# Kernel optimization log

Hardware: AMD Instinct MI355X
Metric: run time of the kernel (lower is better)

## Reference

```python
import jax, jax.numpy as jnp
import numpy as np
from jax import lax

K = 5          # CARAFE kernel_size
S = 2          # scale_factor (downsample stride)
GROUP = 1      # mask groups
ENC_PAD = 1    # (encoder_kernel-1)*dilation//2 with encoder_kernel=3


def _conv2d(x, w, b, stride, padding, dilation=1):
    y = lax.conv_general_dilated(
        x, w, window_strides=(stride, stride),
        padding=[(padding, padding), (padding, padding)],
        rhs_dilation=(dilation, dilation),
        dimension_numbers=('NCHW', 'OIHW', 'NCHW'))
    return y + b[None, :, None, None]


def setup_inputs() -> dict:
    key = jax.random.key(0)
    k1, k2, k3 = jax.random.split(key, 3)
    B, C, H, W = 4, 256, 128, 128
    COMP = 64
    x = jax.random.normal(k1, (B, C, H, W), dtype=jnp.float32)
    # xavier-uniform-ish scale for compressor, std=0.001 for content encoder (as in init_weights)
    w1 = jax.random.normal(k2, (COMP, C, 1, 1), dtype=jnp.float32) * (1.0 / np.sqrt(C))
    b1 = jnp.zeros((COMP,), dtype=jnp.float32)
    w2 = jax.random.normal(k3, (K * K * GROUP, COMP, 3, 3), dtype=jnp.float32) * 0.001
    b2 = jnp.zeros((K * K * GROUP,), dtype=jnp.float32)
    return {"x": x, "w1": w1, "b1": b1, "w2": w2, "b2": b2}


def _carafe_forward(x, w1, b1, w2, b2):
    B, C, H, W = x.shape
    compressed = _conv2d(x, w1, b1, stride=1, padding=0)           # (B, 64, H, W)
    mask = _conv2d(compressed, w2, b2, stride=S, padding=ENC_PAD)   # (B, K*K*G, Ho, Wo)
    Ho, Wo = mask.shape[2], mask.shape[3]
    # kernel_normalizer: softmax over the K*K window per group
    mask = jax.nn.softmax(mask.reshape(B, GROUP, K * K, Ho, Wo), axis=2)
    # feature_reassemble: fused unfold * mask sum — accumulate per kernel tap to
    # avoid materializing the full (B, C, K*K, Ho, Wo) tensor.
    pad = K // 2
    x_pad = jnp.pad(x, ((0, 0), (0, 0), (pad, pad), (pad, pad)))
    Cg = C // GROUP
    out = jnp.zeros((B, GROUP, Cg, Ho, Wo), dtype=x.dtype)
    for i in range(K):
        for j in range(K):
            patch = x_pad[:, :, i:i + S * (Ho - 1) + 1:S, j:j + S * (Wo - 1) + 1:S]
            patch = patch.reshape(B, GROUP, Cg, Ho, Wo)
            out = out + patch * mask[:, :, i * K + j][:, :, None]
    return out.reshape(B, C, Ho, Wo)


def reference(x, w1, b1, w2, b2):
    return _carafe_forward(x, w1, b1, w2, b2)
```

## Files before the change

### kernel.cpp

```cpp
#include <hip/hip_runtime.h>
#include <math.h>

#define BN   4
#define CN   256
#define HN   128
#define WN   128
#define COMP 64
#define KK   25
#define HO   64
#define WO   64

#define TB_OFF    36864
#define XT_OFF    37120
#define WS_NEED   ((size_t)(XT_OFF + (size_t)BN * HN * WN * CN / 2) * 4)

typedef short v8s  __attribute__((ext_vector_type(8)));
typedef float v16f __attribute__((ext_vector_type(16)));

__device__ inline ushort f2bf(float f) {
  unsigned u = __float_as_uint(f);
  return (ushort)((u + 0x7fffu + ((u >> 16) & 1u)) >> 16);
}

__global__ __launch_bounds__(256) void prep_kernel(
    const float* __restrict__ x, const float* __restrict__ w1,
    const float* __restrict__ b1, const float* __restrict__ w2,
    float* __restrict__ ws) {
  const int bid = blockIdx.x;
  const int tid = threadIdx.x;
  if (bid < 4096) {
    __shared__ float st[64][65];
    const int b = bid >> 10, h = (bid >> 3) & 127, bx = bid & 7;
    const int wt = bx & 1, ct = bx >> 1;
    const int w0 = wt * 64, c0 = ct * 64;
    {
      const int wl = tid & 63, cw = tid >> 6;
#pragma unroll
      for (int i = 0; i < 16; ++i) {
        int cl = cw * 16 + i;
        st[cl][wl] = x[((size_t)(b * CN + c0 + cl) * HN + h) * WN + w0 + wl];
      }
    }
    __syncthreads();
    ushort* xT = (ushort*)(ws + XT_OFF);
    const int cg = tid & 15, wl0 = tid >> 4;
#pragma unroll
    for (int wi = 0; wi < 4; ++wi) {
      int wl = wl0 + wi * 16;
      ushort4 o = make_ushort4(f2bf(st[cg * 4 + 0][wl]), f2bf(st[cg * 4 + 1][wl]),
                               f2bf(st[cg * 4 + 2][wl]), f2bf(st[cg * 4 + 3][wl]));
      *(ushort4*)(xT + ((size_t)((b * HN + h) * WN + w0 + wl)) * CN + c0 + cg * 4) = o;
    }
  } else {
    const int cid = bid - 4096;
    const int t = cid >> 2;
    const int chunk = (cid & 3) * 4 + (tid >> 6);
    const int lane = tid & 63;
    const int m = lane & 31, half = lane >> 5;
    const int c0 = chunk * 16 + half * 8;
    float acc[8] = {0.f, 0.f, 0.f, 0.f, 0.f, 0.f, 0.f, 0.f};
    if (m < KK) {
      for (int k = 0; k < COMP; ++k) {
        float wv = w2[(size_t)(m * COMP + k) * 9 + t];
        const float* w1r = w1 + (size_t)k * CN + c0;
        float4 a = *(const float4*)w1r;
        float4 bq = *(const float4*)(w1r + 4);
        acc[0] += wv * a.x;  acc[1] += wv * a.y;
        acc[2] += wv * a.z;  acc[3] += wv * a.w;
        acc[4] += wv * bq.x; acc[5] += wv * bq.y;
        acc[6] += wv * bq.z; acc[7] += wv * bq.w;
      }
    }
    ushort* wA = (ushort*)ws;
    ushort pk[8];
#pragma unroll
    for (int j = 0; j < 8; ++j) pk[j] = f2bf(acc[j]);
    *(ushort4*)(wA + ((size_t)(t * 16 + chunk) * 64 + lane) * 8) =
        make_ushort4(pk[0], pk[1], pk[2], pk[3]);
    *(ushort4*)(wA + ((size_t)(t * 16 + chunk) * 64 + lane) * 8 + 4) =
        make_ushort4(pk[4], pk[5], pk[6], pk[7]);
    if (chunk == 0 && lane < KK) {
      float tbv = 0.f;
      for (int k = 0; k < COMP; ++k)
        tbv += w2[(size_t)(lane * COMP + k) * 9 + t] * b1[k];
      ws[TB_OFF + lane * 9 + t] = tbv;
    }
  }
}

__global__ __launch_bounds__(1024, 4) void conv_softmax_gather(
    const float* __restrict__ ws, const float* __restrict__ b2,
    const float* __restrict__ x, float* __restrict__ out) {
  const int ho = blockIdx.x, b = blockIdx.y;
  const int tid = threadIdx.x;
  const int lane = tid & 63;
  const int wv = tid >> 6;
  const int n = lane & 31, half = lane >> 5;
  const ushort* xT = (const ushort*)(ws + XT_OFF);
  const ushort* wA = (const ushort*)ws;
  const int coff = wv * 16 + half * 8;
  const v8s zero8 = {};
  v16f acc[2] = {{}, {}};

  __shared__ float red[8 * KK * 64];
  __shared__ float sml[KK * 64];

#pragma unroll
  for (int dr = 0; dr < 3; ++dr) {
    const int r = 2 * ho + dr - 1;
    if (r < 0) continue;
#pragma unroll
    for (int dc = 0; dc < 3; ++dc) {
      const int t = dr * 3 + dc;
      const ushort* ap = wA + ((size_t)(t * 16 + wv) * 64 + lane) * 8;
      v8s af = *(const v8s*)ap;
      const size_t rowbase = (size_t)((b * HN + r) * WN);
#pragma unroll
      for (int wt = 0; wt < 2; ++wt) {
        const int wo = wt * 32 + n;
        const int q = 2 * wo + dc - 1;
        const bool bad = q < 0;
        const int qc = bad ? 0 : q;
        const ushort* bp = xT + (rowbase + qc) * CN + coff;
        v8s bf = *(const v8s*)bp;
        if (dc == 0 && bad) bf = zero8;
        acc[wt] = __builtin_amdgcn_mfma_f32_32x32x16_bf16(af, bf, acc[wt], 0, 0, 0);
      }
    }
  }

  const int wo = lane;
  const int c_base = __builtin_amdgcn_readfirstlane(wv * 16);
  const float* __restrict__ xb = x + (size_t)(b * CN) * (HN * WN);
  const int col = 2 * wo;
  float2 g[2][5];
  auto load_g = [&](int ci, float2* dst) {
    const float* xc = xb + (size_t)(c_base + ci) * (HN * WN);
#pragma unroll
    for (int i = 0; i < 5; ++i) {
      int r = 2 * ho - 2 + i;
      dst[i] = (r >= 0 && r < HN) ? *(const float2*)(xc + r * WN + col)
                                  : make_float2(0.f, 0.f);
    }
  };
  load_g(0, g[0]);
  load_g(1, g[1]);

  if (wv >= 8) {
#pragma unroll
    for (int wt = 0; wt < 2; ++wt)
#pragma unroll
      for (int rg = 0; rg < 16; ++rg) {
        int m = (rg & 3) + 8 * (rg >> 2) + 4 * half;
        if (m < KK) red[((wv - 8) * KK + m) * 64 + wt * 32 + n] = acc[wt][rg];
      }
  }
  __syncthreads();
  if (wv < 8) {
#pragma unroll
    for (int wt = 0; wt < 2; ++wt)
#pragma unroll
      for (int rg = 0; rg < 16; ++rg) {
        int m = (rg & 3) + 8 * (rg >> 2) + 4 * half;
        if (m < KK) red[(wv * KK + m) * 64 + wt * 32 + n] += acc[wt][rg];
      }
  }
  __syncthreads();
  if (wv < 4) {
#pragma unroll
    for (int m = 0; m < KK; ++m)
      red[(wv * KK + m) * 64 + wo] += red[((wv + 4) * KK + m) * 64 + wo];
  }
  __syncthreads();
  if (wv < 2) {
#pragma unroll
    for (int m = 0; m < KK; ++m)
      red[(wv * KK + m) * 64 + wo] += red[((wv + 2) * KK + m) * 64 + wo];
  }
  __syncthreads();
  if (tid < 64) {
    const float* tb = ws + TB_OFF;
    const float vr0 = (ho > 0) ? 1.f : 0.f;
    const float vq0 = (wo > 0) ? 1.f : 0.f;
    float logit[KK];
    float mx = -1e30f;
#pragma unroll
    for (int m = 0; m < KK; ++m) {
      const float* t9 = tb + m * 9;
      float l = b2[m]
              + vr0 * (vq0 * t9[0] + t9[1] + t9[2])
              +       (vq0 * t9[3] + t9[4] + t9[5])
              +       (vq0 * t9[6] + t9[7] + t9[8]);
      l += red[(0 * KK + m) * 64 + wo] + red[(1 * KK + m) * 64 + wo];
      logit[m] = l;
      mx = fmaxf(mx, l);
    }
    float ssum = 0.f;
#pragma unroll
    for (int m = 0; m < KK; ++m) {
      float e = __expf(logit[m] - mx);
      logit[m] = e;
      ssum += e;
    }
    float inv = 1.f / ssum;
#pragma unroll
    for (int m = 0; m < KK; ++m) sml[m * 64 + wo] = logit[m] * inv;
  }
  __syncthreads();

  float smr[KK];
#pragma unroll
  for (int m = 0; m < KK; ++m) smr[m] = sml[m * 64 + wo];

  const float wok = (wo > 0) ? 1.f : 0.f;
  const float w63 = (wo < 63) ? 1.f : 0.f;
  for (int ci = 0; ci < 16; ++ci) {
    float2 v[5];
#pragma unroll
    for (int i = 0; i < 5; ++i) v[i] = g[ci & 1][i];
    if (ci + 2 < 16) load_g(ci + 2, g[ci & 1]);

    float acc2 = 0.f;
#pragma unroll
    for (int i = 0; i < 5; ++i) {
      float lx = wok * __shfl_up(v[i].x, 1, 64);
      float ly = wok * __shfl_up(v[i].y, 1, 64);
      float rx = w63 * __shfl_down(v[i].x, 1, 64);
      acc2 += lx * smr[i * 5 + 0] + ly * smr[i * 5 + 1]
            + v[i].x * smr[i * 5 + 2] + v[i].y * smr[i * 5 + 3]
            + rx * smr[i * 5 + 4];
    }
    out[(((size_t)(b * CN + c_base + ci)) * HO + ho) * WO + wo] = acc2;
  }
}

#define FB_WSTRIDE 240
#define FB_TB_OFF  (256 * FB_WSTRIDE)

__global__ __launch_bounds__(256) void compose_w_fb(
    const float* __restrict__ w1, const float* __restrict__ b1,
    const float* __restrict__ w2, float* __restrict__ ws) {
  int mt = blockIdx.x, c = threadIdx.x;
  float acc = 0.f;
#pragma unroll 8
  for (int k = 0; k < COMP; ++k)
    acc += w2[(size_t)(mt / 9 * COMP + k) * 9 + (mt % 9)] * w1[k * CN + c];
  ws[c * FB_WSTRIDE + mt] = acc;
  if (mt < FB_WSTRIDE - 225) ws[c * FB_WSTRIDE + 225 + mt] = 0.f;
  if (c == 0) {
    float tbv = 0.f;
    for (int k = 0; k < COMP; ++k)
      tbv += w2[(size_t)(mt / 9 * COMP + k) * 9 + (mt % 9)] * b1[k];
    ws[FB_TB_OFF + mt] = tbv;
  }
}

__global__ __launch_bounds__(1024, 4) void fused_fb(
    const float* __restrict__ x, const float* __restrict__ b2,
    const float* __restrict__ ws, float* __restrict__ out) {
  const int ho = blockIdx.x, b = blockIdx.y, tid = threadIdx.x;
  const int wo = tid & 63, wv = tid >> 6;
  const int c_base = __builtin_amdgcn_readfirstlane(wv * 16);
  const float* __restrict__ w2c = ws;
  const float* __restrict__ tb  = ws + FB_TB_OFF;
  __shared__ float red[8 * KK * 64];
  __shared__ float sm[KK * 64];
  const float* __restrict__ xb = x + (size_t)(b * CN) * (HN * WN);
  const int col = 2 * wo;
  float acc[KK];
#pragma unroll
  for (int m = 0; m < KK; ++m) acc[m] = 0.f;
  float2 xbuf[2][3];
  auto load_ch = [&](int ci, float2* dst) {
    const float* xc = xb + (size_t)(c_base + ci) * (HN * WN);
    dst[0] = (ho > 0) ? *(const float2*)(xc + (2 * ho - 1) * WN + col)
                      : make_float2(0.f, 0.f);
    dst[1] = *(const float2*)(xc + (2 * ho) * WN + col);
    dst[2] = *(const float2*)(xc + (2 * ho + 1) * WN + col);
  };
  load_ch(0, xbuf[0]);
  load_ch(1, xbuf[1]);
  const float wok = (wo > 0) ? 1.f : 0.f;
  for (int ci = 0; ci < 16; ++ci) {
    float2 r0 = xbuf[ci & 1][0], r1 = xbuf[ci & 1][1], r2 = xbuf[ci & 1][2];
    if (ci + 2 < 16) load_ch(ci + 2, xbuf[ci & 1]);
    float xv[9];
    xv[0] = wok * __shfl_up(r0.y, 1, 64); xv[1] = r0.x; xv[2] = r0.y;
    xv[3] = wok * __shfl_up(r1.y, 1, 64); xv[4] = r1.x; xv[5] = r1.y;
    xv[6] = wok * __shfl_up(r2.y, 1, 64); xv[7] = r2.x; xv[8] = r2.y;
    const float* __restrict__ wrow = w2c + (size_t)(c_base + ci) * FB_WSTRIDE;
#pragma unroll
    for (int m = 0; m < KK; ++m) {
      float a = acc[m];
#pragma unroll
      for (int t = 0; t < 9; ++t) a += wrow[m * 9 + t] * xv[t];
      acc[m] = a;
    }
  }
  float2 g[2][5];
  auto load_g = [&](int ci, float2* dst) {
    const float* xc = xb + (size_t)(c_base + ci) * (HN * WN);
#pragma unroll
    for (int i = 0; i < 5; ++i) {
      int r = 2 * ho - 2 + i;
      dst[i] = (r >= 0 && r < HN) ? *(const float2*)(xc + r * WN + col)
                                  : make_float2(0.f, 0.f);
    }
  };
  load_g(0, g[0]);
  load_g(1, g[1]);
  if (wv >= 8) {
#pragma unroll
    for (int m = 0; m < KK; ++m) red[((wv - 8) * KK + m) * 64 + wo] = acc[m];
  }
  __syncthreads();
  if (wv < 8) {
#pragma unroll
    for (int m = 0; m < KK; ++m) red[(wv * KK + m) * 64 + wo] += acc[m];
  }
  __syncthreads();
  if (wv < 4) {
#pragma unroll
    for (int m = 0; m < KK; ++m)
      red[(wv * KK + m) * 64 + wo] += red[((wv + 4) * KK + m) * 64 + wo];
  }
  __syncthreads();
  if (wv < 2) {
#pragma unroll
    for (int m = 0; m < KK; ++m)
      red[(wv * KK + m) * 64 + wo] += red[((wv + 2) * KK + m) * 64 + wo];
  }
  __syncthreads();
  if (tid < 64) {
    const float vr0 = (ho > 0) ? 1.f : 0.f;
    const float vq0 = (wo > 0) ? 1.f : 0.f;
    float logit[KK];
    float mx = -1e30f;
#pragma unroll
    for (int m = 0; m < KK; ++m) {
      const float* t9 = tb + m * 9;
      float l = b2[m]
              + vr0 * (vq0 * t9[0] + t9[1] + t9[2])
              +       (vq0 * t9[3] + t9[4] + t9[5])
              +       (vq0 * t9[6] + t9[7] + t9[8]);
      l += red[(0 * KK + m) * 64 + wo] + red[(1 * KK + m) * 64 + wo];
      logit[m] = l;
      mx = fmaxf(mx, l);
    }
    float s = 0.f;
#pragma unroll
    for (int m = 0; m < KK; ++m) {
      float e = __expf(logit[m] - mx);
      logit[m] = e;
      s += e;
    }
    float inv = 1.f / s;
#pragma unroll
    for (int m = 0; m < KK; ++m) sm[m * 64 + wo] = logit[m] * inv;
  }
  __syncthreads();
  float smr[KK];
#pragma unroll
  for (int m = 0; m < KK; ++m) smr[m] = sm[m * 64 + wo];
  const float w63 = (wo < 63) ? 1.f : 0.f;
  for (int ci = 0; ci < 16; ++ci) {
    float2 v[5];
#pragma unroll
    for (int i = 0; i < 5; ++i) v[i] = g[ci & 1][i];
    if (ci + 2 < 16) load_g(ci + 2, g[ci & 1]);
    float acc2 = 0.f;
#pragma unroll
    for (int i = 0; i < 5; ++i) {
      float lx = wok * __shfl_up(v[i].x, 1, 64);
      float ly = wok * __shfl_up(v[i].y, 1, 64);
      float rx = w63 * __shfl_down(v[i].x, 1, 64);
      acc2 += lx * smr[i * 5 + 0] + ly * smr[i * 5 + 1]
            + v[i].x * smr[i * 5 + 2] + v[i].y * smr[i * 5 + 3]
            + rx * smr[i * 5 + 4];
    }
    out[(((size_t)(b * CN + c_base + ci)) * HO + ho) * WO + wo] = acc2;
  }
}

extern "C" void kernel_launch(void* const* d_in, const int* in_sizes, int n_in,
                              void* d_out, int out_size, void* d_ws, size_t ws_size,
                              hipStream_t stream) {
  const float* x  = (const float*)d_in[0];
  const float* w1 = (const float*)d_in[1];
  const float* b1 = (const float*)d_in[2];
  const float* w2 = (const float*)d_in[3];
  const float* b2 = (const float*)d_in[4];
  float* out = (float*)d_out;
  float* ws  = (float*)d_ws;

  if (ws_size >= WS_NEED) {
    hipLaunchKernelGGL(prep_kernel, dim3(4096 + 36), dim3(256), 0, stream,
                       x, w1, b1, w2, ws);
    hipLaunchKernelGGL(conv_softmax_gather, dim3(HO, BN), dim3(1024), 0, stream,
                       ws, b2, x, out);
  } else {
    hipLaunchKernelGGL(compose_w_fb, dim3(225), dim3(256), 0, stream,
                       w1, b1, w2, ws);
    hipLaunchKernelGGL(fused_fb, dim3(HO, BN), dim3(1024), 0, stream,
                       x, b2, ws, out);
  }
}
```

Before: 160.0 us.

## Stage bf16 transposed input rows in LDS instead of a global prep pass

Drops the separate pass that transposed and converted all of x into a bf16 channel-last workspace buffer. The main kernel now loads the three input rows it needs per output row in 64-channel chunks, converts them to bf16, and writes them into swizzled shared memory. MFMA B operands are read from there, with register prefetch of the next chunk overlapping the current chunk's MFMAs. This removes a full read-and-write round trip of x through HBM, at the cost of extra block barriers, more LDS use that may reduce occupancy, and redundant reads of overlapping rows across blocks.

Result: faster. 149.0 us (-6.9%).

```diff
diff --git a/kernel.cpp b/kernel.cpp
--- a/kernel.cpp
+++ b/kernel.cpp
@@ -11,8 +11,7 @@
 #define WO   64
 
 #define TB_OFF    36864
-#define XT_OFF    37120
-#define WS_NEED   ((size_t)(XT_OFF + (size_t)BN * HN * WN * CN / 2) * 4)
+#define WS_NEED   ((size_t)(TB_OFF + 256) * 4)
 
 typedef short v8s  __attribute__((ext_vector_type(8)));
 typedef float v16f __attribute__((ext_vector_type(16)));
@@ -22,73 +21,46 @@
   return (ushort)((u + 0x7fffu + ((u >> 16) & 1u)) >> 16);
 }
 
-__global__ __launch_bounds__(256) void prep_kernel(
-    const float* __restrict__ x, const float* __restrict__ w1,
-    const float* __restrict__ b1, const float* __restrict__ w2,
-    float* __restrict__ ws) {
-  const int bid = blockIdx.x;
+__global__ __launch_bounds__(256) void compose_kernel(
+    const float* __restrict__ w1, const float* __restrict__ b1,
+    const float* __restrict__ w2, float* __restrict__ ws) {
+  const int cid = blockIdx.x;
   const int tid = threadIdx.x;
-  if (bid < 4096) {
-    __shared__ float st[64][65];
-    const int b = bid >> 10, h = (bid >> 3) & 127, bx = bid & 7;
-    const int wt = bx & 1, ct = bx >> 1;
-    const int w0 = wt * 64, c0 = ct * 64;
-    {
-      const int wl = tid & 63, cw = tid >> 6;
-#pragma unroll
-      for (int i = 0; i < 16; ++i) {
-        int cl = cw * 16 + i;
-        st[cl][wl] = x[((size_t)(b * CN + c0 + cl) * HN + h) * WN + w0 + wl];
-      }
-    }
-    __syncthreads();
-    ushort* xT = (ushort*)(ws + XT_OFF);
-    const int cg = tid & 15, wl0 = tid >> 4;
-#pragma unroll
-    for (int wi = 0; wi < 4; ++wi) {
-      int wl = wl0 + wi * 16;
-      ushort4 o = make_ushort4(f2bf(st[cg * 4 + 0][wl]), f2bf(st[cg * 4 + 1][wl]),
-                               f2bf(st[cg * 4 + 2][wl]), f2bf(st[cg * 4 + 3][wl]));
-      *(ushort4*)(xT + ((size_t)((b * HN + h) * WN + w0 + wl)) * CN + c0 + cg * 4) = o;
-    }
-  } else {
-    const int cid = bid - 4096;
-    const int t = cid >> 2;
-    const int chunk = (cid & 3) * 4 + (tid >> 6);
-    const int lane = tid & 63;
-    const int m = lane & 31, half = lane >> 5;
-    const int c0 = chunk * 16 + half * 8;
-    float acc[8] = {0.f, 0.f, 0.f, 0.f, 0.f, 0.f, 0.f, 0.f};
-    if (m < KK) {
-      for (int k = 0; k < COMP; ++k) {
-        float wv = w2[(size_t)(m * COMP + k) * 9 + t];
-        const float* w1r = w1 + (size_t)k * CN + c0;
-        float4 a = *(const float4*)w1r;
-        float4 bq = *(const float4*)(w1r + 4);
-        acc[0] += wv * a.x;  acc[1] += wv * a.y;
-        acc[2] += wv * a.z;  acc[3] += wv * a.w;
-        acc[4] += wv * bq.x; acc[5] += wv * bq.y;
-        acc[6] += wv * bq.z; acc[7] += wv * bq.w;
-      }
-    }
-    ushort* wA = (ushort*)ws;
-    ushort pk[8];
-#pragma unroll
-    for (int j = 0; j < 8; ++j) pk[j] = f2bf(acc[j]);
-    *(ushort4*)(wA + ((size_t)(t * 16 + chunk) * 64 + lane) * 8) =
-        make_ushort4(pk[0], pk[1], pk[2], pk[3]);
-    *(ushort4*)(wA + ((size_t)(t * 16 + chunk) * 64 + lane) * 8 + 4) =
-        make_ushort4(pk[4], pk[5], pk[6], pk[7]);
-    if (chunk == 0 && lane < KK) {
-      float tbv = 0.f;
-      for (int k = 0; k < COMP; ++k)
-        tbv += w2[(size_t)(lane * COMP + k) * 9 + t] * b1[k];
-      ws[TB_OFF + lane * 9 + t] = tbv;
-    }
-  }
-}
-
-__global__ __launch_bounds__(1024, 4) void conv_softmax_gather(
+  const int t = cid >> 2;
+  const int chunk = (cid & 3) * 4 + (tid >> 6);
+  const int lane = tid & 63;
+  const int m = lane & 31, half = lane >> 5;
+  const int c0 = chunk * 16 + half * 8;
+  float acc[8] = {0.f, 0.f, 0.f, 0.f, 0.f, 0.f, 0.f, 0.f};
+  if (m < KK) {
+    for (int k = 0; k < COMP; ++k) {
+      float wv = w2[(size_t)(m * COMP + k) * 9 + t];
+      const float* w1r = w1 + (size_t)k * CN + c0;
+      float4 a = *(const float4*)w1r;
+      float4 bq = *(const float4*)(w1r + 4);
+      acc[0] += wv * a.x;  acc[1] += wv * a.y;
+      acc[2] += wv * a.z;  acc[3] += wv * a.w;
+      acc[4] += wv * bq.x; acc[5] += wv * bq.y;
+      acc[6] += wv * bq.z; acc[7] += wv * bq.w;
+    }
+  }
+  ushort* wA = (ushort*)ws;
+  ushort pk[8];
+#pragma unroll
+  for (int j = 0; j < 8; ++j) pk[j] = f2bf(acc[j]);
+  *(ushort4*)(wA + ((size_t)(t * 16 + chunk) * 64 + lane) * 8) =
+      make_ushort4(pk[0], pk[1], pk[2], pk[3]);
+  *(ushort4*)(wA + ((size_t)(t * 16 + chunk) * 64 + lane) * 8 + 4) =
+      make_ushort4(pk[4], pk[5], pk[6], pk[7]);
+  if (chunk == 0 && lane < KK) {
+    float tbv = 0.f;
+    for (int k = 0; k < COMP; ++k)
+      tbv += w2[(size_t)(lane * COMP + k) * 9 + t] * b1[k];
+    ws[TB_OFF + lane * 9 + t] = tbv;
+  }
+}
+
+__global__ __launch_bounds__(1024, 4) void fused_main(
     const float* __restrict__ ws, const float* __restrict__ b2,
     const float* __restrict__ x, float* __restrict__ out) {
   const int ho = blockIdx.x, b = blockIdx.y;
@@ -96,33 +68,71 @@
   const int lane = tid & 63;
   const int wv = tid >> 6;
   const int n = lane & 31, half = lane >> 5;
-  const ushort* xT = (const ushort*)(ws + XT_OFF);
+
+  __shared__ __attribute__((aligned(16))) char smem[57600];
+  float* red = (float*)smem;
+  float* sml = (float*)(smem + 51200);
+
   const ushort* wA = (const ushort*)ws;
-  const int coff = wv * 16 + half * 8;
+  const float* __restrict__ xb = x + (size_t)(b * CN) * (HN * WN);
+
+  const int px = tid & 127;
+  const int cg = tid >> 7;
+  float sreg[3][8];
+
+  auto stage_load = [&](int c) {
+#pragma unroll
+    for (int dr = 0; dr < 3; ++dr) {
+      const int r = 2 * ho + dr - 1;
+      if (r >= 0) {
+        const float* xp = xb + ((size_t)(c * 64 + cg * 8) * HN + r) * WN + px;
+#pragma unroll
+        for (int i = 0; i < 8; ++i) sreg[dr][i] = xp[(size_t)i * (HN * WN)];
+      } else {
+#pragma unroll
+        for (int i = 0; i < 8; ++i) sreg[dr][i] = 0.f;
+      }
+    }
+  };
+  auto stage_write = [&]() {
+#pragma unroll
+    for (int dr = 0; dr < 3; ++dr) {
+      v8s o;
+#pragma unroll
+      for (int i = 0; i < 8; ++i) o[i] = (short)f2bf(sreg[dr][i]);
+      const int boff = (((dr * 128 + px) * 64 + cg * 8) * 2)
+                       ^ (((px >> 1) & 7) << 4);
+      *(v8s*)(smem + boff) = o;
+    }
+  };
+
+  const int kf = wv & 3;
+  const int tg = wv >> 2;
   const v8s zero8 = {};
   v16f acc[2] = {{}, {}};
 
-  __shared__ float red[8 * KK * 64];
-  __shared__ float sml[KK * 64];
-
-#pragma unroll
-  for (int dr = 0; dr < 3; ++dr) {
-    const int r = 2 * ho + dr - 1;
-    if (r < 0) continue;
-#pragma unroll
-    for (int dc = 0; dc < 3; ++dc) {
-      const int t = dr * 3 + dc;
-      const ushort* ap = wA + ((size_t)(t * 16 + wv) * 64 + lane) * 8;
-      v8s af = *(const v8s*)ap;
-      const size_t rowbase = (size_t)((b * HN + r) * WN);
+  stage_load(0);
+  for (int c = 0; c < 4; ++c) {
+    __syncthreads();
+    stage_write();
+    __syncthreads();
+    if (c < 3) stage_load(c + 1);
+    const int kidx = c * 4 + kf;
+#pragma unroll
+    for (int t = 0; t < 9; ++t) {
+      const int tgt = (t >= 6) ? 3 : (t >> 1);
+      if (tgt != tg) continue;
+      const int dr = t / 3, dc = t % 3;
+      if (2 * ho + dr - 1 < 0) continue;
+      const v8s af = *(const v8s*)(wA + ((size_t)(t * 16 + kidx) * 64 + lane) * 8);
 #pragma unroll
       for (int wt = 0; wt < 2; ++wt) {
-        const int wo = wt * 32 + n;
-        const int q = 2 * wo + dc - 1;
+        const int q = 2 * (wt * 32 + n) + dc - 1;
         const bool bad = q < 0;
         const int qc = bad ? 0 : q;
-        const ushort* bp = xT + (rowbase + qc) * CN + coff;
-        v8s bf = *(const v8s*)bp;
+        const int boff = (((dr * 128 + qc) * 64 + kf * 16 + half * 8) * 2)
+                         ^ (((qc >> 1) & 7) << 4);
+        v8s bf = *(const v8s*)(smem + boff);
         if (dc == 0 && bad) bf = zero8;
         acc[wt] = __builtin_amdgcn_mfma_f32_32x32x16_bf16(af, bf, acc[wt], 0, 0, 0);
       }
@@ -131,7 +141,6 @@
 
   const int wo = lane;
   const int c_base = __builtin_amdgcn_readfirstlane(wv * 16);
-  const float* __restrict__ xb = x + (size_t)(b * CN) * (HN * WN);
   const int col = 2 * wo;
   float2 g[2][5];
   auto load_g = [&](int ci, float2* dst) {
@@ -145,6 +154,8 @@
   };
   load_g(0, g[0]);
   load_g(1, g[1]);
+
+  __syncthreads();
 
   if (wv >= 8) {
 #pragma unroll
@@ -394,9 +405,9 @@
   float* ws  = (float*)d_ws;
 
   if (ws_size >= WS_NEED) {
-    hipLaunchKernelGGL(prep_kernel, dim3(4096 + 36), dim3(256), 0, stream,
-                       x, w1, b1, w2, ws);
-    hipLaunchKernelGGL(conv_softmax_gather, dim3(HO, BN), dim3(1024), 0, stream,
+    hipLaunchKernelGGL(compose_kernel, dim3(36), dim3(256), 0, stream,
+                       w1, b1, w2, ws);
+    hipLaunchKernelGGL(fused_main, dim3(HO, BN), dim3(1024), 0, stream,
                        ws, b2, x, out);
   } else {
     hipLaunchKernelGGL(compose_w_fb, dim3(225), dim3(256), 0, stream,
```

## Compute 1x1 compression explicitly and split pipeline into compress, mask, gather kernels

Applied to the files above, without the earlier changes.

Replaces the pre-composed w2·w1 weights and the full bf16 transpose of x with an explicit 1x1 compression GEMM (MFMA) that writes a 64-channel bf16 intermediate. A separate kernel stages that intermediate in swizzled LDS, runs the 3x3 stride-2 conv and softmax, and writes the mask to the workspace. The gather becomes its own kernel with 256 threads and a remapped grid. The intent is to cut the 256-channel transpose traffic and the 9x-wider composed GEMM, at the cost of extra launches and a round trip of the mask and compressed tensor through global memory.

Measured after the change: 147.6 us. -7.8%, faster.

```diff
diff --git a/kernel.cpp b/kernel.cpp
--- a/kernel.cpp
+++ b/kernel.cpp
@@ -10,9 +10,11 @@
 #define HO   64
 #define WO   64
 
-#define TB_OFF    36864
-#define XT_OFF    37120
-#define WS_NEED   ((size_t)(XT_OFF + (size_t)BN * HN * WN * CN / 2) * 4)
+#define W1B_OFF  0
+#define W2A_OFF  8192
+#define MASK_OFF 17408
+#define COMP_OFF 427008
+#define WS_NEED  ((size_t)(COMP_OFF + (size_t)BN * HN * WN * COMP / 2) * 4)
 
 typedef short v8s  __attribute__((ext_vector_type(8)));
 typedef float v16f __attribute__((ext_vector_type(16)));
@@ -22,116 +24,181 @@
   return (ushort)((u + 0x7fffu + ((u >> 16) & 1u)) >> 16);
 }
 
-__global__ __launch_bounds__(256) void prep_kernel(
-    const float* __restrict__ x, const float* __restrict__ w1,
-    const float* __restrict__ b1, const float* __restrict__ w2,
+__global__ __launch_bounds__(64) void compose_frags(
+    const float* __restrict__ w1, const float* __restrict__ w2,
     float* __restrict__ ws) {
   const int bid = blockIdx.x;
+  const int lane = threadIdx.x;
+  const int k0 = (lane >> 5) * 8;
+  ushort pk[8];
+  ushort* dst;
+  if (bid < 32) {
+    const int kidx = bid >> 1, nt = bid & 1;
+    const int ch = nt * 32 + (lane & 31);
+    const int c0 = kidx * 16 + k0;
+#pragma unroll
+    for (int j = 0; j < 8; ++j) pk[j] = f2bf(w1[(size_t)ch * CN + c0 + j]);
+    dst = (ushort*)(ws + W1B_OFF) + ((size_t)((kidx * 2 + nt) * 64 + lane)) * 8;
+  } else {
+    const int g = bid - 32;
+    const int t = g >> 2, kidx = g & 3;
+    const int m = lane & 31;
+    const int kk0 = kidx * 16 + k0;
+#pragma unroll
+    for (int j = 0; j < 8; ++j) {
+      float v = (m < KK) ? w2[((size_t)(m * COMP + kk0 + j)) * 9 + t] : 0.f;
+      pk[j] = f2bf(v);
+    }
+    dst = (ushort*)(ws + W2A_OFF) + ((size_t)((t * 4 + kidx) * 64 + lane)) * 8;
+  }
+  *(ushort4*)(dst)     = make_ushort4(pk[0], pk[1], pk[2], pk[3]);
+  *(ushort4*)(dst + 4) = make_ushort4(pk[4], pk[5], pk[6], pk[7]);
+}
+
+__global__ __launch_bounds__(256, 4) void compress_kernel(
+    const float* __restrict__ x, const float* __restrict__ b1,
+    float* __restrict__ ws) {
+  const int h = blockIdx.x, b = blockIdx.y;
   const int tid = threadIdx.x;
-  if (bid < 4096) {
-    __shared__ float st[64][65];
-    const int b = bid >> 10, h = (bid >> 3) & 127, bx = bid & 7;
-    const int wt = bx & 1, ct = bx >> 1;
-    const int w0 = wt * 64, c0 = ct * 64;
-    {
-      const int wl = tid & 63, cw = tid >> 6;
-#pragma unroll
-      for (int i = 0; i < 16; ++i) {
-        int cl = cw * 16 + i;
-        st[cl][wl] = x[((size_t)(b * CN + c0 + cl) * HN + h) * WN + w0 + wl];
-      }
-    }
-    __syncthreads();
-    ushort* xT = (ushort*)(ws + XT_OFF);
-    const int cg = tid & 15, wl0 = tid >> 4;
-#pragma unroll
-    for (int wi = 0; wi < 4; ++wi) {
-      int wl = wl0 + wi * 16;
-      ushort4 o = make_ushort4(f2bf(st[cg * 4 + 0][wl]), f2bf(st[cg * 4 + 1][wl]),
-                               f2bf(st[cg * 4 + 2][wl]), f2bf(st[cg * 4 + 3][wl]));
-      *(ushort4*)(xT + ((size_t)((b * HN + h) * WN + w0 + wl)) * CN + c0 + cg * 4) = o;
-    }
-  } else {
-    const int cid = bid - 4096;
-    const int t = cid >> 2;
-    const int chunk = (cid & 3) * 4 + (tid >> 6);
-    const int lane = tid & 63;
-    const int m = lane & 31, half = lane >> 5;
-    const int c0 = chunk * 16 + half * 8;
-    float acc[8] = {0.f, 0.f, 0.f, 0.f, 0.f, 0.f, 0.f, 0.f};
-    if (m < KK) {
-      for (int k = 0; k < COMP; ++k) {
-        float wv = w2[(size_t)(m * COMP + k) * 9 + t];
-        const float* w1r = w1 + (size_t)k * CN + c0;
-        float4 a = *(const float4*)w1r;
-        float4 bq = *(const float4*)(w1r + 4);
-        acc[0] += wv * a.x;  acc[1] += wv * a.y;
-        acc[2] += wv * a.z;  acc[3] += wv * a.w;
-        acc[4] += wv * bq.x; acc[5] += wv * bq.y;
-        acc[6] += wv * bq.z; acc[7] += wv * bq.w;
-      }
-    }
-    ushort* wA = (ushort*)ws;
-    ushort pk[8];
-#pragma unroll
-    for (int j = 0; j < 8; ++j) pk[j] = f2bf(acc[j]);
-    *(ushort4*)(wA + ((size_t)(t * 16 + chunk) * 64 + lane) * 8) =
-        make_ushort4(pk[0], pk[1], pk[2], pk[3]);
-    *(ushort4*)(wA + ((size_t)(t * 16 + chunk) * 64 + lane) * 8 + 4) =
-        make_ushort4(pk[4], pk[5], pk[6], pk[7]);
-    if (chunk == 0 && lane < KK) {
-      float tbv = 0.f;
-      for (int k = 0; k < COMP; ++k)
-        tbv += w2[(size_t)(lane * COMP + k) * 9 + t] * b1[k];
-      ws[TB_OFF + lane * 9 + t] = tbv;
-    }
-  }
-}
-
-__global__ __launch_bounds__(1024, 4) void conv_softmax_gather(
-    const float* __restrict__ ws, const float* __restrict__ b2,
-    const float* __restrict__ x, float* __restrict__ out) {
+  const int lane = tid & 63, w = tid >> 6;
+  const int nn = lane & 31, kh = lane >> 5;
+  const int px = w * 32 + nn;
+  const ushort* w1B = (const ushort*)(ws + W1B_OFF);
+  v16f acc[2] = {{}, {}};
+#pragma unroll 2
+  for (int kidx = 0; kidx < 16; ++kidx) {
+    const float* xc = x + (((size_t)(b * CN + kidx * 16 + kh * 8)) * HN + h) * WN + px;
+    float av[8];
+#pragma unroll
+    for (int j = 0; j < 8; ++j) av[j] = xc[(size_t)j * (HN * WN)];
+    v8s af;
+#pragma unroll
+    for (int j = 0; j < 8; ++j) af[j] = (short)f2bf(av[j]);
+    v8s bf0 = *(const v8s*)(w1B + ((size_t)((kidx * 2 + 0) * 64 + lane)) * 8);
+    v8s bf1 = *(const v8s*)(w1B + ((size_t)((kidx * 2 + 1) * 64 + lane)) * 8);
+    acc[0] = __builtin_amdgcn_mfma_f32_32x32x16_bf16(af, bf0, acc[0], 0, 0, 0);
+    acc[1] = __builtin_amdgcn_mfma_f32_32x32x16_bf16(af, bf1, acc[1], 0, 0, 0);
+  }
+  ushort* comp = (ushort*)(ws + COMP_OFF);
+  const size_t rowbase = (size_t)(b * HN + h) * WN;
+#pragma unroll
+  for (int nt = 0; nt < 2; ++nt) {
+    const float bias = b1[nt * 32 + nn];
+#pragma unroll
+    for (int rg = 0; rg < 16; ++rg) {
+      const int pr = w * 32 + (rg & 3) + 8 * (rg >> 2) + 4 * kh;
+      comp[(rowbase + pr) * COMP + nt * 32 + nn] = f2bf(acc[nt][rg] + bias);
+    }
+  }
+}
+
+#define MS_LDS 49152
+__global__ __launch_bounds__(256, 4) void mask_softmax(
+    const float* __restrict__ b2, float* __restrict__ ws) {
   const int ho = blockIdx.x, b = blockIdx.y;
   const int tid = threadIdx.x;
-  const int lane = tid & 63;
-  const int wv = tid >> 6;
-  const int n = lane & 31, half = lane >> 5;
-  const ushort* xT = (const ushort*)(ws + XT_OFF);
-  const ushort* wA = (const ushort*)ws;
-  const int coff = wv * 16 + half * 8;
+  const int lane = tid & 63, w = tid >> 6;
+  __shared__ __attribute__((aligned(16))) char smem[MS_LDS];
+  float* red = (float*)smem;
+  const ushort* comp = (const ushort*)(ws + COMP_OFF);
+
+#pragma unroll
+  for (int i = 0; i < 12; ++i) {
+    const int flat = i * 256 + tid;
+    const int r = flat >> 10;
+    const int px = (flat >> 3) & 127;
+    const int cg = flat & 7;
+    const int rr = 2 * ho + r - 1;
+    v8s v = {};
+    if (rr >= 0)
+      v = *(const v8s*)(comp + ((size_t)(b * HN + rr) * WN + px) * COMP + cg * 8);
+    const int boff = (((r * 128 + px) * 64 + cg * 8) * 2) ^ (((px >> 1) & 7) << 4);
+    *(v8s*)(smem + boff) = v;
+  }
+  __syncthreads();
+
+  const int nt = w & 1, kh2 = w >> 1;
+  const int nn = lane & 31;
+  const ushort* w2A = (const ushort*)(ws + W2A_OFF);
   const v8s zero8 = {};
-  v16f acc[2] = {{}, {}};
-
-  __shared__ float red[8 * KK * 64];
+  v16f acc = {};
+#pragma unroll
+  for (int t = 0; t < 9; ++t) {
+    const int dr = t / 3, dc = t % 3;
+#pragma unroll
+    for (int ki = 0; ki < 2; ++ki) {
+      const int kidx = kh2 * 2 + ki;
+      const v8s af = *(const v8s*)(w2A + ((size_t)((t * 4 + kidx) * 64 + lane)) * 8);
+      const int q = 2 * (nt * 32 + nn) + dc - 1;
+      const bool bad = q < 0;
+      const int qc = bad ? 0 : q;
+      const int boff = (((dr * 128 + qc) * 64 + kidx * 16 + (lane >> 5) * 8) * 2)
+                       ^ (((qc >> 1) & 7) << 4);
+      v8s bf = *(const v8s*)(smem + boff);
+      if (dc == 0 && bad) bf = zero8;
+      acc = __builtin_amdgcn_mfma_f32_32x32x16_bf16(af, bf, acc, 0, 0, 0);
+    }
+  }
+  __syncthreads();
+
+  if (kh2 == 1) {
+#pragma unroll
+    for (int rg = 0; rg < 16; ++rg) {
+      const int m = (rg & 3) + 8 * (rg >> 2) + 4 * (lane >> 5);
+      if (m < KK) red[(nt * KK + m) * 32 + nn] = acc[rg];
+    }
+  }
+  __syncthreads();
+  if (kh2 == 0) {
+#pragma unroll
+    for (int rg = 0; rg < 16; ++rg) {
+      const int m = (rg & 3) + 8 * (rg >> 2) + 4 * (lane >> 5);
+      if (m < KK) red[(nt * KK + m) * 32 + nn] += acc[rg];
+    }
+  }
+  __syncthreads();
+
+  if (tid < 64) {
+    const int wo = tid;
+    const int tnt = wo >> 5, tc = wo & 31;
+    float logit[KK];
+    float mx = -1e30f;
+#pragma unroll
+    for (int m = 0; m < KK; ++m) {
+      float l = b2[m] + red[(tnt * KK + m) * 32 + tc];
+      logit[m] = l;
+      mx = fmaxf(mx, l);
+    }
+    float ssum = 0.f;
+#pragma unroll
+    for (int m = 0; m < KK; ++m) {
+      float e = __expf(logit[m] - mx);
+      logit[m] = e;
+      ssum += e;
+    }
+    const float inv = 1.f / ssum;
+    float* mdst = ws + MASK_OFF + (size_t)(b * HO + ho) * KK * 64;
+#pragma unroll
+    for (int m = 0; m < KK; ++m) mdst[m * 64 + wo] = logit[m] * inv;
+  }
+}
+
+__global__ __launch_bounds__(256, 4) void gather_kernel(
+    const float* __restrict__ ws, const float* __restrict__ x,
+    float* __restrict__ out) {
+  const int bid0 = blockIdx.x;
+  const int bid = (bid0 & 7) * 128 + (bid0 >> 3);
+  const int ho = bid & 63;
+  const int cq = (bid >> 6) & 3;
+  const int b = bid >> 8;
+  const int tid = threadIdx.x;
+  const int lane = tid & 63, wv = tid >> 6;
+
   __shared__ float sml[KK * 64];
 
-#pragma unroll
-  for (int dr = 0; dr < 3; ++dr) {
-    const int r = 2 * ho + dr - 1;
-    if (r < 0) continue;
-#pragma unroll
-    for (int dc = 0; dc < 3; ++dc) {
-      const int t = dr * 3 + dc;
-      const ushort* ap = wA + ((size_t)(t * 16 + wv) * 64 + lane) * 8;
-      v8s af = *(const v8s*)ap;
-      const size_t rowbase = (size_t)((b * HN + r) * WN);
-#pragma unroll
-      for (int wt = 0; wt < 2; ++wt) {
-        const int wo = wt * 32 + n;
-        const int q = 2 * wo + dc - 1;
-        const bool bad = q < 0;
-        const int qc = bad ? 0 : q;
-        const ushort* bp = xT + (rowbase + qc) * CN + coff;
-        v8s bf = *(const v8s*)bp;
-        if (dc == 0 && bad) bf = zero8;
-        acc[wt] = __builtin_amdgcn_mfma_f32_32x32x16_bf16(af, bf, acc[wt], 0, 0, 0);
-      }
-    }
-  }
-
+  const float* __restrict__ xb = x + (size_t)(b * CN) * (HN * WN);
   const int wo = lane;
-  const int c_base = __builtin_amdgcn_readfirstlane(wv * 16);
-  const float* __restrict__ xb = x + (size_t)(b * CN) * (HN * WN);
+  const int c_base = __builtin_amdgcn_readfirstlane(cq * 64 + wv * 16);
   const int col = 2 * wo;
   float2 g[2][5];
   auto load_g = [&](int ci, float2* dst) {
@@ -146,66 +213,8 @@
   load_g(0, g[0]);
   load_g(1, g[1]);
 
-  if (wv >= 8) {
-#pragma unroll
-    for (int wt = 0; wt < 2; ++wt)
-#pragma unroll
-      for (int rg = 0; rg < 16; ++rg) {
-        int m = (rg & 3) + 8 * (rg >> 2) + 4 * half;
-        if (m < KK) red[((wv - 8) * KK + m) * 64 + wt * 32 + n] = acc[wt][rg];
-      }
-  }
-  __syncthreads();
-  if (wv < 8) {
-#pragma unroll
-    for (int wt = 0; wt < 2; ++wt)
-#pragma unroll
-      for (int rg = 0; rg < 16; ++rg) {
-        int m = (rg & 3) + 8 * (rg >> 2) + 4 * half;
-        if (m < KK) red[(wv * KK + m) * 64 + wt * 32 + n] += acc[wt][rg];
-      }
-  }
-  __syncthreads();
-  if (wv < 4) {
-#pragma unroll
-    for (int m = 0; m < KK; ++m)
-      red[(wv * KK + m) * 64 + wo] += red[((wv + 4) * KK + m) * 64 + wo];
-  }
-  __syncthreads();
-  if (wv < 2) {
-#pragma unroll
-    for (int m = 0; m < KK; ++m)
-      red[(wv * KK + m) * 64 + wo] += red[((wv + 2) * KK + m) * 64 + wo];
-  }
-  __syncthreads();
-  if (tid < 64) {
-    const float* tb = ws + TB_OFF;
-    const float vr0 = (ho > 0) ? 1.f : 0.f;
-    const float vq0 = (wo > 0) ? 1.f : 0.f;
-    float logit[KK];
-    float mx = -1e30f;
-#pragma unroll
-    for (int m = 0; m < KK; ++m) {
-      const float* t9 = tb + m * 9;
-      float l = b2[m]
-              + vr0 * (vq0 * t9[0] + t9[1] + t9[2])
-              +       (vq0 * t9[3] + t9[4] + t9[5])
-              +       (vq0 * t9[6] + t9[7] + t9[8]);
-      l += red[(0 * KK + m) * 64 + wo] + red[(1 * KK + m) * 64 + wo];
-      logit[m] = l;
-      mx = fmaxf(mx, l);
-    }
-    float ssum = 0.f;
-#pragma unroll
-    for (int m = 0; m < KK; ++m) {
-      float e = __expf(logit[m] - mx);
-      logit[m] = e;
-      ssum += e;
-    }
-    float inv = 1.f / ssum;
-#pragma unroll
-    for (int m = 0; m < KK; ++m) sml[m * 64 + wo] = logit[m] * inv;
-  }
+  const float* msrc = ws + MASK_OFF + (size_t)(b * HO + ho) * KK * 64;
+  for (int i = tid; i < KK * 64; i += 256) sml[i] = msrc[i];
   __syncthreads();
 
   float smr[KK];
@@ -394,10 +403,14 @@
   float* ws  = (float*)d_ws;
 
   if (ws_size >= WS_NEED) {
-    hipLaunchKernelGGL(prep_kernel, dim3(4096 + 36), dim3(256), 0, stream,
-                       x, w1, b1, w2, ws);
-    hipLaunchKernelGGL(conv_softmax_gather, dim3(HO, BN), dim3(1024), 0, stream,
-                       ws, b2, x, out);
+    hipLaunchKernelGGL(compose_frags, dim3(68), dim3(64), 0, stream,
+                       w1, w2, ws);
+    hipLaunchKernelGGL(compress_kernel, dim3(HN, BN), dim3(256), 0, stream,
+                       x, b1, ws);
+    hipLaunchKernelGGL(mask_softmax, dim3(HO, BN), dim3(256), 0, stream,
+                       b2, ws);
+    hipLaunchKernelGGL(gather_kernel, dim3(1024), dim3(256), 0, stream,
+                       ws, x, out);
   } else {
     hipLaunchKernelGGL(compose_w_fb, dim3(225), dim3(256), 0, stream,
                        w1, b1, w2, ws);
```
